# Optimization experiments

Hardware: AMD Instinct MI355X
Metric: run time of the kernel (lower is better)

Reference implementation:

```python
import jax, jax.numpy as jnp
import numpy as np

B, L, D = 4, 2048, 768
K, M, CK = 12, 1, 4            # heads, thetas, conv kernel size
H = D // (K * M)               # 64
DIM_MEM = K * H                # 768
DIM_EXPAND = H * 3             # 192
DSH = DIM_EXPAND * 2           # 384 swiglu head dim
DST = K * DSH                  # 4608
DIM_FUSED = DIM_MEM + K + DST  # 5388
THETA_MIN, THETA_MAX = 1e-3, 3.0


def setup_inputs() -> dict:
    key = jax.random.key(0)
    ks = jax.random.split(key, 5)
    x = jax.random.normal(ks[0], (B, L, D), jnp.float32)
    W_in = jax.random.normal(ks[1], (D, DIM_FUSED), jnp.float32) * 0.02
    conv_w = jax.random.normal(ks[2], (CK, DIM_MEM + K), jnp.float32) * 0.2  # depthwise taps
    rms_scale = jnp.ones((H,), jnp.float32)
    # theta_raw init (M==1 branch): inverse-sigmoid of geomspace grid
    grid = np.geomspace(THETA_MIN, THETA_MAX, K).reshape(1, 1, K, 1, 1)
    base = np.tile(grid, (1, 1, 1, H, 1))
    u = np.clip((base - THETA_MIN) / (THETA_MAX - THETA_MIN), 1e-4, 1 - 1e-4)
    theta_raw = jnp.asarray(np.log(u) - np.log(1.0 - u), jnp.float32)
    decay_slopes = jnp.asarray(np.log(np.exp(np.geomspace(1e-3, 0.1, K)) - 1.0), jnp.float32)
    score_scale = jnp.ones((K,), jnp.float32)
    tanh_scale = jnp.ones((K,), jnp.float32)
    W_sw = jax.random.normal(ks[3], (2 * K * H * M, DST), jnp.float32) * 0.02
    W_out = jax.random.normal(ks[4], (K * DIM_EXPAND, D), jnp.float32) * 0.02
    return {"x": x, "W_in": W_in, "conv_w": conv_w, "rms_scale": rms_scale,
            "theta_raw": theta_raw, "decay_slopes": decay_slopes,
            "score_scale": score_scale, "tanh_scale": tanh_scale,
            "W_sw": W_sw, "W_out": W_out}


def reference(x, W_in, conv_w, rms_scale, theta_raw, decay_slopes,
              score_scale, tanh_scale, W_sw, W_out):
    # fused in-projection
    z_fused = jnp.einsum('bld,df->blf', x, W_in)
    z_mem = z_fused[..., :DIM_MEM + K]
    skip_direct = z_fused[..., DIM_MEM + K:]
    # causal depthwise conv (kernel size CK, left pad CK-1)
    zp = jnp.pad(z_mem, ((0, 0), (CK - 1, 0), (0, 0)))
    z_conv = sum(zp[:, j:j + L, :] * conv_w[j] for j in range(CK))
    z_mem = jax.nn.silu(z_conv)
    # memory keys + RMSNorm over H
    k_val = z_mem[..., :DIM_MEM].reshape(B, L, K, H)
    k_val = k_val * jax.lax.rsqrt(jnp.mean(k_val * k_val, axis=-1, keepdims=True) + 1e-6) * rms_scale
    s_raw = z_mem[..., DIM_MEM:]  # (B, L, K)
    # theta (M == 1)
    theta = THETA_MIN + (THETA_MAX - THETA_MIN) * jax.nn.sigmoid(theta_raw)  # (1,1,K,H,1)
    # decay time weights (num_anchor_heads == 0, maxlen == L)
    pos = jnp.arange(L, dtype=jnp.float32)
    slopes = jax.nn.softplus(decay_slopes).reshape(1, 1, K)
    dist = jnp.maximum(jnp.float32(L - 1) - pos, 0.0)
    log_time_weight = -slopes * dist[None, :, None]  # (1, L, K)
    log_p = jnp.clip(score_scale[None, None, :] * s_raw, -10.0, 10.0)
    p_w = jnp.exp(log_p + log_time_weight)  # (B, L, K)
    # characteristic-function encoding
    k5 = k_val[..., None]  # (B, L, K, H, 1)
    phi = jnp.tanh(k5 * tanh_scale.reshape(1, 1, K, 1, 1)) * theta
    kvw = k5 * p_w[..., None, None]
    re = kvw * jnp.cos(phi)
    im = kvw * jnp.sin(phi)
    # fused causal cumulative accumulation
    flat = K * H * M
    stack = jnp.concatenate([p_w, re.reshape(B, L, flat), im.reshape(B, L, flat)], axis=-1)
    cs = jnp.cumsum(stack, axis=1)
    den_acc = cs[..., :K]
    re_acc = cs[..., K:K + flat].reshape(B, L, K, H, M)
    im_acc = cs[..., K + flat:].reshape(B, L, K, H, M)
    inv_den = (1.0 / jnp.maximum(den_acc, 1e-4))[..., None, None]
    summary_flat = jnp.stack([re_acc * inv_den, im_acc * inv_den], axis=-1).reshape(B, L, -1)
    # SwiGLU with skip
    y_spectral = jnp.einsum('bls,sf->blf', summary_flat, W_sw).reshape(B, L, K, DSH)
    y_skip = skip_direct.reshape(B, L, K, DSH)
    y_spec_val, y_spec_gate = jnp.split(y_spectral, 2, axis=-1)
    y_skip_val, y_skip_gate = jnp.split(y_skip, 2, axis=-1)
    y_act = (y_spec_val + y_skip_val) * jax.nn.silu(y_spec_gate + y_skip_gate)
    out = jnp.einsum('blf,fd->bld', y_act.reshape(B, L, -1), W_out)
    return out
```

## Files before the change

### kernel.cpp

```cpp
#include <hip/hip_runtime.h>
#include <hip/hip_bf16.h>

#define B_       4
#define L_       2048
#define D_       768
#define K_       12
#define H_       64
#define CK_      4
#define DIM_MEM_ 768
#define DMK      780
#define NT       (B_*L_)
#define NSUM     1536
#define NACT     2304
#define NCHUNK   16
#define CHLEN    (L_/NCHUNK)
#define PSTRIDE  132

typedef __attribute__((ext_vector_type(8))) short          bf16x8;
typedef __attribute__((ext_vector_type(8))) unsigned short u16x8;
typedef __attribute__((ext_vector_type(4))) float          f32x4;

__device__ __forceinline__ ushort f2bf(float v) {
    __hip_bfloat16 h = __float2bfloat16(v);
    return *reinterpret_cast<ushort*>(&h);
}
__device__ __forceinline__ float tanh_fast(float x) {
    float t = __expf(-2.f * fabsf(x));
    float r = (1.f - t) / (1.f + t);
    return copysignf(r, x);
}

struct PrepJobs {
    const float* W[6];
    ushort*      out[6];
    int ldw[6], Kd[6], colbase[6], remap[6], ntx[6];
    int start[7];
    const float* cast_in;
    ushort*      cast_out;
    int n4;
};

__global__ __launch_bounds__(256)
void prep_all(PrepJobs J)
{
    int blk = blockIdx.x;
    if (blk >= J.start[6]) {
        int i = (blk - J.start[6]) * 256 + threadIdx.x;
        if (i < J.n4) {
            float4 v = reinterpret_cast<const float4*>(J.cast_in)[i];
            ushort4 o;
            o.x = f2bf(v.x); o.y = f2bf(v.y); o.z = f2bf(v.z); o.w = f2bf(v.w);
            reinterpret_cast<ushort4*>(J.cast_out)[i] = o;
        }
        return;
    }
    int j = 0;
    while (blk >= J.start[j + 1]) ++j;
    int rel = blk - J.start[j];
    int ntx = J.ntx[j];
    int n0 = (rel % ntx) * 32, k0 = (rel / ntx) * 32;
    const float* W = J.W[j];
    int ldw = J.ldw[j], Kd = J.Kd[j], colbase = J.colbase[j], remap = J.remap[j];
    ushort* out = J.out[j];

    __shared__ float tile[32][33];
    int tx = threadIdx.x & 31, ty = threadIdx.x >> 5;
    int n = n0 + tx;
    int c;
    if (remap) {
        int grp = n >> 5, which = (n >> 4) & 1, nn = (grp << 4) + (n & 15);
        c = colbase + (nn / 192) * 384 + which * 192 + (nn % 192);
    } else {
        c = colbase + n;
    }
    #pragma unroll
    for (int r = 0; r < 4; ++r)
        tile[ty + r*8][tx] = W[(size_t)(k0 + ty + r*8) * ldw + c];
    __syncthreads();
    #pragma unroll
    for (int r = 0; r < 4; ++r)
        out[(size_t)(n0 + ty + r*8) * Kd + k0 + tx] = f2bf(tile[tx][ty + r*8]);
}

__global__ __launch_bounds__(256)
void gemm_bf16_mfma(const ushort* __restrict__ A, const ushort* __restrict__ BT,
                    float* __restrict__ C, int Kd, int N, int ldc)
{
    __shared__ ushort As[128*64];
    __shared__ ushort Bs[128*64];
    int tid = threadIdx.x, lane = tid & 63;
    int lr = lane & 15, quad = lane >> 4;
    int wave = tid >> 6;
    int wr = (wave >> 1) * 64, wc = (wave & 1) * 64;
    int m0 = blockIdx.y * 128, n0 = blockIdx.x * 128;

    f32x4 acc[4][4] = {};

    int srow = tid >> 3;
    int tc   = tid & 7;
    const ushort* gA = A  + (size_t)(m0 + srow) * Kd + tc * 8;
    const ushort* gB = BT + (size_t)(n0 + srow) * Kd + tc * 8;
    int woff = srow * 64 + ((tc ^ (srow & 7)) * 8);
    int rx = lr & 7;

    for (int k0 = 0; k0 < Kd; k0 += 64) {
        u16x8 a[4], b[4];
        #pragma unroll
        for (int p = 0; p < 4; ++p) {
            a[p] = *reinterpret_cast<const u16x8*>(gA + (size_t)(32*p) * Kd);
            b[p] = *reinterpret_cast<const u16x8*>(gB + (size_t)(32*p) * Kd);
        }
        gA += 64; gB += 64;
        __syncthreads();
        #pragma unroll
        for (int p = 0; p < 4; ++p) {
            *reinterpret_cast<u16x8*>(As + woff + p*2048) = a[p];
            *reinterpret_cast<u16x8*>(Bs + woff + p*2048) = b[p];
        }
        __syncthreads();
        #pragma unroll
        for (int ks = 0; ks < 2; ++ks) {
            bf16x8 af[4], bf[4];
            #pragma unroll
            for (int i = 0; i < 4; ++i) {
                int ca = ((ks*4 + quad) ^ rx) * 8;
                af[i] = *reinterpret_cast<const bf16x8*>(As + (wr + i*16 + lr) * 64 + ca);
                bf[i] = *reinterpret_cast<const bf16x8*>(Bs + (wc + i*16 + lr) * 64 + ca);
            }
            #pragma unroll
            for (int i = 0; i < 4; ++i)
                #pragma unroll
                for (int j = 0; j < 4; ++j)
                    acc[i][j] = __builtin_amdgcn_mfma_f32_16x16x32_bf16(
                                    af[i], bf[j], acc[i][j], 0, 0, 0);
        }
    }

    #pragma unroll
    for (int i = 0; i < 4; ++i)
        #pragma unroll
        for (int j = 0; j < 4; ++j)
            #pragma unroll
            for (int r = 0; r < 4; ++r) {
                int row = m0 + wr + i*16 + quad*4 + r;
                int col = n0 + wc + j*16 + lr;
                if (col < N)
                    C[(size_t)row * ldc + col] = acc[i][j][r];
            }
}

#define G2NKT 36

#define GLOAD16(gp, dp) __builtin_amdgcn_global_load_lds( \
    (__attribute__((address_space(1))) const void*)(gp),  \
    (__attribute__((address_space(3))) void*)(dp), 16, 0, 0)

__device__ __forceinline__ void g2_stageA(ushort* lds_, int kt,
                                          const ushort* pAs, const ushort* pAx,
                                          int wave, int part)
{
    int ktc = kt > (G2NKT-1) ? (G2NKT-1) : kt;
    const ushort* g; size_t kd;
    if (ktc < 24) { g = pAs + ktc*64;      kd = 1536; }
    else          { g = pAx + (ktc-24)*64; kd = 768;  }
    g += (size_t)(part * 64) * kd;
    ushort* d = lds_ + (kt & 1) * 8192 + part * 4096 + wave * 512;
    GLOAD16(g,           d);
    GLOAD16(g + 32*kd,   d + 2048);
}

__device__ __forceinline__ void g2_stageB(ushort* lds_, int kt,
                                          const ushort* pBs, const ushort* pBx,
                                          int wave)
{
    int ktc = kt > (G2NKT-1) ? (G2NKT-1) : kt;
    const ushort* g; size_t kd;
    if (ktc < 24) { g = pBs + ktc*64;      kd = 1536; }
    else          { g = pBx + (ktc-24)*64; kd = 768;  }
    ushort* d = lds_ + 16384 + (kt & 1) * 12288 + wave * 512;
    #pragma unroll
    for (int s = 0; s < 6; ++s)
        GLOAD16(g + (size_t)(32*s)*kd, d + 2048*s);
}

__global__ __launch_bounds__(256, 2)
void gemm2_2blk(const ushort* __restrict__ Sm, const ushort* __restrict__ Xb,
                const ushort* __restrict__ WsC, const ushort* __restrict__ WiC,
                ushort* __restrict__ yact)
{
    __shared__ ushort lds[40960];
    const int tid  = threadIdx.x;
    const int lane = tid & 63, wave = tid >> 6;
    const int lr = lane & 15, quad = lane >> 4, rx = lr & 7;
    const int wr = (wave >> 1) * 64;
    const int wc = (wave & 1) * 96;
    const int m0 = blockIdx.y * 128, n0 = blockIdx.x * 192;

    const int sr = tid >> 3;
    const int sc = (tid & 7) ^ (sr & 7);
    const ushort* pAs = Sm  + (size_t)(m0 + sr) * 1536 + sc * 8;
    const ushort* pAx = Xb  + (size_t)(m0 + sr) * 768  + sc * 8;
    const ushort* pBs = WsC + (size_t)(n0 + sr) * 1536 + sc * 8;
    const ushort* pBx = WiC + (size_t)(n0 + sr) * 768  + sc * 8;

    f32x4 acc[4][6] = {};
    bf16x8 af[4][2];
    const int ca0 = (quad ^ rx) * 8;
    const int ca1 = ((4 + quad) ^ rx) * 8;

    g2_stageA(lds, 0, pAs, pAx, wave, 0);
    g2_stageA(lds, 0, pAs, pAx, wave, 1);
    g2_stageB(lds, 0, pBs, pBx, wave);
    g2_stageA(lds, 1, pAs, pAx, wave, 0);
    g2_stageA(lds, 1, pAs, pAx, wave, 1);
    asm volatile("s_waitcnt vmcnt(4)" ::: "memory");
    __builtin_amdgcn_s_barrier();

    #pragma unroll 1
    for (int g = 0; g < G2NKT; ++g) {
        const ushort* Ab = lds + (g & 1) * 8192;
        const ushort* Bb = lds + 16384 + (g & 1) * 12288;

        {
            #pragma unroll
            for (int i = 0; i < 4; ++i) {
                const ushort* p = Ab + (wr + i*16 + lr) * 64;
                af[i][0] = *reinterpret_cast<const bf16x8*>(p + ca0);
                af[i][1] = *reinterpret_cast<const bf16x8*>(p + ca1);
            }
            bf16x8 bfr[2][2];
            #pragma unroll
            for (int j = 0; j < 2; ++j) {
                const ushort* p = Bb + (wc + j*16 + lr) * 64;
                bfr[j][0] = *reinterpret_cast<const bf16x8*>(p + ca0);
                bfr[j][1] = *reinterpret_cast<const bf16x8*>(p + ca1);
            }
            g2_stageB(lds, g + 1, pBs, pBx, wave);
            __builtin_amdgcn_s_barrier();
            asm volatile("s_waitcnt lgkmcnt(0)" ::: "memory");
            __builtin_amdgcn_sched_barrier(0);
            __builtin_amdgcn_s_setprio(1);
            #pragma unroll
            for (int ks = 0; ks < 2; ++ks)
                #pragma unroll
                for (int i = 0; i < 4; ++i)
                    #pragma unroll
                    for (int j = 0; j < 2; ++j)
                        acc[i][j] = __builtin_amdgcn_mfma_f32_16x16x32_bf16(
                                        af[i][ks], bfr[j][ks], acc[i][j], 0, 0, 0);
            __builtin_amdgcn_s_setprio(0);
            __builtin_amdgcn_s_barrier();
        }
        {
            bf16x8 bfr[2][2];
            #pragma unroll
            for (int j = 0; j < 2; ++j) {
                const ushort* p = Bb + (wc + (2 + j)*16 + lr) * 64;
                bfr[j][0] = *reinterpret_cast<const bf16x8*>(p + ca0);
                bfr[j][1] = *reinterpret_cast<const bf16x8*>(p + ca1);
            }
            g2_stageA(lds, g + 2, pAs, pAx, wave, 0);
            __builtin_amdgcn_s_barrier();
            asm volatile("s_waitcnt lgkmcnt(0)" ::: "memory");
            __builtin_amdgcn_sched_barrier(0);
            __builtin_amdgcn_s_setprio(1);
            #pragma unroll
            for (int ks = 0; ks < 2; ++ks)
                #pragma unroll
                for (int i = 0; i < 4; ++i)
                    #pragma unroll
                    for (int j = 0; j < 2; ++j)
                        acc[i][2 + j] = __builtin_amdgcn_mfma_f32_16x16x32_bf16(
                                        af[i][ks], bfr[j][ks], acc[i][2 + j], 0, 0, 0);
            __builtin_amdgcn_s_setprio(0);
            __builtin_amdgcn_s_barrier();
        }
        {
            bf16x8 bfr[2][2];
            #pragma unroll
            for (int j = 0; j < 2; ++j) {
                const ushort* p = Bb + (wc + (4 + j)*16 + lr) * 64;
                bfr[j][0] = *reinterpret_cast<const bf16x8*>(p + ca0);
                bfr[j][1] = *reinterpret_cast<const bf16x8*>(p + ca1);
            }
            g2_stageA(lds, g + 2, pAs, pAx, wave, 1);
            asm volatile("s_waitcnt vmcnt(4)" ::: "memory");
            __builtin_amdgcn_s_barrier();
            asm volatile("s_waitcnt lgkmcnt(0)" ::: "memory");
            __builtin_amdgcn_sched_barrier(0);
            __builtin_amdgcn_s_setprio(1);
            #pragma unroll
            for (int ks = 0; ks < 2; ++ks)
                #pragma unroll
                for (int i = 0; i < 4; ++i)
                    #pragma unroll
                    for (int j = 0; j < 2; ++j)
                        acc[i][4 + j] = __builtin_amdgcn_mfma_f32_16x16x32_bf16(
                                        af[i][ks], bfr[j][ks], acc[i][4 + j], 0, 0, 0);
            __builtin_amdgcn_s_setprio(0);
            __builtin_amdgcn_s_barrier();
        }
    }
    asm volatile("s_waitcnt vmcnt(0)" ::: "memory");

    const int vg0 = (n0 + wc) >> 5;
    #pragma unroll
    for (int i = 0; i < 4; ++i)
        #pragma unroll
        for (int p = 0; p < 3; ++p)
            #pragma unroll
            for (int r = 0; r < 4; ++r) {
                int row = m0 + wr + i*16 + quad*4 + r;
                int col = (vg0 + p)*16 + lr;
                float v  = acc[i][2*p][r];
                float gt = acc[i][2*p + 1][r];
                float y = v * (gt / (1.f + __expf(-gt)));
                yact[(size_t)row * NACT + col] = f2bf(y);
            }
}

__global__ __launch_bounds__(256)
void token_kernel(const float* __restrict__ zmem, const float* __restrict__ conv_w,
                  const float* __restrict__ rms_scale, const float* __restrict__ theta_raw,
                  const float* __restrict__ dslopes, const float* __restrict__ sscale,
                  const float* __restrict__ tscale,
                  float* __restrict__ pw, float* __restrict__ re, float* __restrict__ im)
{
    int t = blockIdx.x;
    int b = t >> 11;
    int l = t & (L_ - 1);
    int tid = threadIdx.x;
    int h = tid & 63, kg = tid >> 6;

    __shared__ float s_pw[K_];

    if (tid < K_) {
        float acc = 0.f;
        #pragma unroll
        for (int j = 0; j < CK_; ++j) {
            int ll = l - (CK_ - 1) + j;
            if (ll >= 0)
                acc += zmem[(size_t)(b*L_ + ll)*DMK + DIM_MEM_ + tid]
                     * conv_w[j*DMK + DIM_MEM_ + tid];
        }
        float s  = acc / (1.f + expf(-acc));
        float lp = sscale[tid] * s;
        lp = fminf(10.f, fmaxf(-10.f, lp));
        float slope = log1pf(expf(dslopes[tid]));
        s_pw[tid] = expf(lp - slope * (float)(L_ - 1 - l));
    }

    float kv[3];
    #pragma unroll
    for (int q = 0; q < 3; ++q) {
        int kk = kg + q*4;
        int c = kk*H_ + h;
        float acc = 0.f;
        #pragma unroll
        for (int j = 0; j < CK_; ++j) {
            int ll = l - (CK_ - 1) + j;
            if (ll >= 0)
                acc += zmem[(size_t)(b*L_ + ll)*DMK + c] * conv_w[j*DMK + c];
        }
        kv[q] = acc / (1.f + __expf(-acc));
    }
    __syncthreads();

    #pragma unroll
    for (int q = 0; q < 3; ++q) {
        int kk = kg + q*4;
        float v = kv[q];
        float ss = v * v;
        #pragma unroll
        for (int off = 32; off > 0; off >>= 1)
            ss += __shfl_xor(ss, off, 64);
        float kn = v * rsqrtf(ss * (1.f/64.f) + 1e-6f) * rms_scale[h];
        float th = 0.001f + 2.999f * (1.f / (1.f + __expf(-theta_raw[kk*H_ + h])));
        float phi = tanh_fast(kn * tscale[kk]) * th;
        float kvw = kn * s_pw[kk];
        re[(size_t)t*(K_*H_) + kk*H_ + h] = kvw * __cosf(phi);
        im[(size_t)t*(K_*H_) + kk*H_ + h] = kvw * __sinf(phi);
    }
    if (tid < K_) pw[(size_t)t*K_ + tid] = s_pw[tid];
}

__global__ __launch_bounds__(128)
void scan_sums(const float* __restrict__ pw, const float* __restrict__ re,
               const float* __restrict__ im, float* __restrict__ part)
{
    int blk = blockIdx.x;
    int chunk = blk & (NCHUNK - 1);
    int bk = blk >> 4;
    int k = bk % K_;
    int b = bk / K_;
    int tid = threadIdx.x;
    int h = tid & 63;
    const float* __restrict__ src = (tid >> 6) ? im : re;
    int l0 = chunk * CHLEN;

    size_t base  = ((size_t)(b*L_ + l0))*(K_*H_) + k*H_ + h;
    size_t dbase = ((size_t)(b*L_ + l0))*K_ + k;
    float s = 0.f, ds = 0.f;
    for (int i0 = 0; i0 < CHLEN; i0 += 8) {
        float v[8], d[8];
        #pragma unroll
        for (int j = 0; j < 8; ++j) {
            v[j] = src[base + (size_t)(i0 + j)*(K_*H_)];
            d[j] = pw [dbase + (size_t)(i0 + j)*K_];
        }
        #pragma unroll
        for (int j = 0; j < 8; ++j) { s += v[j]; ds += d[j]; }
    }
    size_t pb = ((size_t)bk * NCHUNK + chunk) * PSTRIDE;
    part[pb + tid] = s;
    if (tid == 0) part[pb + 128] = ds;
}

__global__ __launch_bounds__(128)
void scan_final(const float* __restrict__ pw, const float* __restrict__ re,
                const float* __restrict__ im, const float* __restrict__ part,
                ushort* __restrict__ summary)
{
    int blk = blockIdx.x;
    int chunk = blk & (NCHUNK - 1);
    int bk = blk >> 4;
    int k = bk % K_;
    int b = bk / K_;
    int tid = threadIdx.x;
    int h = tid & 63;
    int pi = tid >> 6;
    const float* __restrict__ src = pi ? im : re;
    int l0 = chunk * CHLEN;

    float acc = 0.f, dacc = 0.f;
    size_t pb0 = (size_t)bk * NCHUNK * PSTRIDE;
    for (int cn = 0; cn < chunk; ++cn) {
        acc  += part[pb0 + (size_t)cn*PSTRIDE + tid];
        dacc += part[pb0 + (size_t)cn*PSTRIDE + 128];
    }

    size_t base  = ((size_t)(b*L_ + l0))*(K_*H_) + k*H_ + h;
    size_t dbase = ((size_t)(b*L_ + l0))*K_ + k;
    int outch = 2*(k*H_ + h) + pi;
    for (int i0 = 0; i0 < CHLEN; i0 += 8) {
        float v[8], d[8];
        #pragma unroll
        for (int j = 0; j < 8; ++j) {
            v[j] = src[base + (size_t)(i0 + j)*(K_*H_)];
            d[j] = pw [dbase + (size_t)(i0 + j)*K_];
        }
        #pragma unroll
        for (int j = 0; j < 8; ++j) {
            acc += v[j]; dacc += d[j];
            float inv = 1.f / fmaxf(dacc, 1e-4f);
            summary[((size_t)(b*L_ + l0 + i0 + j))*NSUM + outch] = f2bf(acc * inv);
        }
    }
}

extern "C" void kernel_launch(void* const* d_in, const int* in_sizes, int n_in,
                              void* d_out, int out_size, void* d_ws, size_t ws_size,
                              hipStream_t stream)
{
    const float* x         = (const float*)d_in[0];
    const float* W_in      = (const float*)d_in[1];
    const float* conv_w    = (const float*)d_in[2];
    const float* rms_scale = (const float*)d_in[3];
    const float* theta_raw = (const float*)d_in[4];
    const float* dslopes   = (const float*)d_in[5];
    const float* sscale    = (const float*)d_in[6];
    const float* tscale    = (const float*)d_in[7];
    const float* W_sw      = (const float*)d_in[8];
    const float* W_out     = (const float*)d_in[9];
    float* out = (float*)d_out;
    char* ws   = (char*)d_ws;

    float*  zmem    = (float*) (ws + 0);
    ushort* summary = (ushort*)(ws + 0);
    float*  pw      = (float*) (ws + 25559040);
    float*  re      = (float*) (ws + 25952256);
    float*  im      = (float*) (ws + 51118080);
    ushort* yact    = (ushort*)(ws + 25952256);
    float*  part    = (float*) (ws + 76283904);
    ushort* xb      = (ushort*)(ws + 76689408);
    ushort* WiCat   = (ushort*)(ws + 89272320);
    ushort* WsCat   = (ushort*)(ws + 96350208);
    ushort* WoT     = (ushort*)(ws + 110505984);
    ushort* WimT    = (ushort*)(ws + 114044928);

    PrepJobs J{};
    J.W[0]=W_in;  J.out[0]=WiCat; J.ldw[0]=5388; J.Kd[0]=768;  J.colbase[0]=780; J.remap[0]=1; J.ntx[0]=144;
    J.W[1]=W_sw;  J.out[1]=WsCat; J.ldw[1]=4608; J.Kd[1]=1536; J.colbase[1]=0;   J.remap[1]=1; J.ntx[1]=144;
    J.W[2]=W_out; J.out[2]=WoT;   J.ldw[2]=768;  J.Kd[2]=2304; J.colbase[2]=0;   J.remap[2]=0; J.ntx[2]=24;
    J.W[3]=W_in;  J.out[3]=WimT;  J.ldw[3]=5388; J.Kd[3]=768;  J.colbase[3]=0;   J.remap[3]=0; J.ntx[3]=28;
    int tiles[4] = {144*24, 144*48, 24*72, 28*24};
    J.start[0] = 0;
    for (int j = 0; j < 4; ++j) J.start[j+1] = J.start[j] + tiles[j];
    J.start[5] = J.start[4];
    J.start[6] = J.start[4];
    J.cast_in = x; J.cast_out = xb; J.n4 = NT*D_/4;
    int nblk = J.start[6] + (J.n4 + 255)/256;

    dim3 blk(256);
    prep_all<<<dim3(nblk), blk, 0, stream>>>(J);
    gemm_bf16_mfma<<<dim3(7, 64), blk, 0, stream>>>(xb, WimT, zmem, 768, 780, 780);
    token_kernel<<<dim3(NT), blk, 0, stream>>>(zmem, conv_w, rms_scale, theta_raw,
                                               dslopes, sscale, tscale, pw, re, im);
    scan_sums <<<dim3(B_*K_*NCHUNK), dim3(128), 0, stream>>>(pw, re, im, part);
    scan_final<<<dim3(B_*K_*NCHUNK), dim3(128), 0, stream>>>(pw, re, im, part, summary);
    gemm2_2blk<<<dim3(24, 64), dim3(256), 0, stream>>>(summary, xb, WsCat, WiCat, yact);
    gemm_bf16_mfma<<<dim3(6, 64), blk, 0, stream>>>(yact, WoT, out, 2304, 768, 768);
}
```

Baseline: 409.7 us.

## Replace three-phase interleaved pipeline in SwiGLU GEMM with single-phase double buffering

The main GEMM loop used to be split into three sub-phases, each with its own barriers and staggered global-to-LDS prefetches. It now issues all prefetches for the next tile up front, reads all A and B fragments from LDS, runs the full MFMA block, then waits on global loads and barriers once per iteration. This removes several barriers per iteration and simplifies the schedule. The cost is shallower prefetch (one tile ahead instead of partly two), a full vmcnt(0) wait on each iteration, and more live B-fragment registers, which could hurt latency hiding or occupancy.

```diff
diff --git a/kernel.cpp b/kernel.cpp
--- a/kernel.cpp
+++ b/kernel.cpp
@@ -184,9 +184,9 @@
 }
 
 __global__ __launch_bounds__(256, 2)
-void gemm2_2blk(const ushort* __restrict__ Sm, const ushort* __restrict__ Xb,
-                const ushort* __restrict__ WsC, const ushort* __restrict__ WiC,
-                ushort* __restrict__ yact)
+void gemm2_1ph(const ushort* __restrict__ Sm, const ushort* __restrict__ Xb,
+               const ushort* __restrict__ WsC, const ushort* __restrict__ WiC,
+               ushort* __restrict__ yact)
 {
     __shared__ ushort lds[40960];
     const int tid  = threadIdx.x;
@@ -204,16 +204,13 @@
     const ushort* pBx = WiC + (size_t)(n0 + sr) * 768  + sc * 8;
 
     f32x4 acc[4][6] = {};
-    bf16x8 af[4][2];
     const int ca0 = (quad ^ rx) * 8;
     const int ca1 = ((4 + quad) ^ rx) * 8;
 
     g2_stageA(lds, 0, pAs, pAx, wave, 0);
     g2_stageA(lds, 0, pAs, pAx, wave, 1);
     g2_stageB(lds, 0, pBs, pBx, wave);
-    g2_stageA(lds, 1, pAs, pAx, wave, 0);
-    g2_stageA(lds, 1, pAs, pAx, wave, 1);
-    asm volatile("s_waitcnt vmcnt(4)" ::: "memory");
+    asm volatile("s_waitcnt vmcnt(0)" ::: "memory");
     __builtin_amdgcn_s_barrier();
 
     #pragma unroll 1
@@ -221,87 +218,37 @@
         const ushort* Ab = lds + (g & 1) * 8192;
         const ushort* Bb = lds + 16384 + (g & 1) * 12288;
 
-        {
+        g2_stageA(lds, g + 1, pAs, pAx, wave, 0);
+        g2_stageA(lds, g + 1, pAs, pAx, wave, 1);
+        g2_stageB(lds, g + 1, pBs, pBx, wave);
+
+        bf16x8 af[4][2], bfr[6][2];
+        #pragma unroll
+        for (int i = 0; i < 4; ++i) {
+            const ushort* p = Ab + (wr + i*16 + lr) * 64;
+            af[i][0] = *reinterpret_cast<const bf16x8*>(p + ca0);
+            af[i][1] = *reinterpret_cast<const bf16x8*>(p + ca1);
+        }
+        #pragma unroll
+        for (int j = 0; j < 6; ++j) {
+            const ushort* p = Bb + (wc + j*16 + lr) * 64;
+            bfr[j][0] = *reinterpret_cast<const bf16x8*>(p + ca0);
+            bfr[j][1] = *reinterpret_cast<const bf16x8*>(p + ca1);
+        }
+        __builtin_amdgcn_s_setprio(1);
+        #pragma unroll
+        for (int ks = 0; ks < 2; ++ks)
             #pragma unroll
-            for (int i = 0; i < 4; ++i) {
-                const ushort* p = Ab + (wr + i*16 + lr) * 64;
-                af[i][0] = *reinterpret_cast<const bf16x8*>(p + ca0);
-                af[i][1] = *reinterpret_cast<const bf16x8*>(p + ca1);
-            }
-            bf16x8 bfr[2][2];
-            #pragma unroll
-            for (int j = 0; j < 2; ++j) {
-                const ushort* p = Bb + (wc + j*16 + lr) * 64;
-                bfr[j][0] = *reinterpret_cast<const bf16x8*>(p + ca0);
-                bfr[j][1] = *reinterpret_cast<const bf16x8*>(p + ca1);
-            }
-            g2_stageB(lds, g + 1, pBs, pBx, wave);
-            __builtin_amdgcn_s_barrier();
-            asm volatile("s_waitcnt lgkmcnt(0)" ::: "memory");
-            __builtin_amdgcn_sched_barrier(0);
-            __builtin_amdgcn_s_setprio(1);
-            #pragma unroll
-            for (int ks = 0; ks < 2; ++ks)
+            for (int i = 0; i < 4; ++i)
                 #pragma unroll
-                for (int i = 0; i < 4; ++i)
-                    #pragma unroll
-                    for (int j = 0; j < 2; ++j)
-                        acc[i][j] = __builtin_amdgcn_mfma_f32_16x16x32_bf16(
-                                        af[i][ks], bfr[j][ks], acc[i][j], 0, 0, 0);
-            __builtin_amdgcn_s_setprio(0);
-            __builtin_amdgcn_s_barrier();
-        }
-        {
-            bf16x8 bfr[2][2];
-            #pragma unroll
-            for (int j = 0; j < 2; ++j) {
-                const ushort* p = Bb + (wc + (2 + j)*16 + lr) * 64;
-                bfr[j][0] = *reinterpret_cast<const bf16x8*>(p + ca0);
-                bfr[j][1] = *reinterpret_cast<const bf16x8*>(p + ca1);
-            }
-            g2_stageA(lds, g + 2, pAs, pAx, wave, 0);
-            __builtin_amdgcn_s_barrier();
-            asm volatile("s_waitcnt lgkmcnt(0)" ::: "memory");
-            __builtin_amdgcn_sched_barrier(0);
-            __builtin_amdgcn_s_setprio(1);
-            #pragma unroll
-            for (int ks = 0; ks < 2; ++ks)
-                #pragma unroll
-                for (int i = 0; i < 4; ++i)
-                    #pragma unroll
-                    for (int j = 0; j < 2; ++j)
-                        acc[i][2 + j] = __builtin_amdgcn_mfma_f32_16x16x32_bf16(
-                                        af[i][ks], bfr[j][ks], acc[i][2 + j], 0, 0, 0);
-            __builtin_amdgcn_s_setprio(0);
-            __builtin_amdgcn_s_barrier();
-        }
-        {
-            bf16x8 bfr[2][2];
-            #pragma unroll
-            for (int j = 0; j < 2; ++j) {
-                const ushort* p = Bb + (wc + (4 + j)*16 + lr) * 64;
-                bfr[j][0] = *reinterpret_cast<const bf16x8*>(p + ca0);
-                bfr[j][1] = *reinterpret_cast<const bf16x8*>(p + ca1);
-            }
-            g2_stageA(lds, g + 2, pAs, pAx, wave, 1);
-            asm volatile("s_waitcnt vmcnt(4)" ::: "memory");
-            __builtin_amdgcn_s_barrier();
-            asm volatile("s_waitcnt lgkmcnt(0)" ::: "memory");
-            __builtin_amdgcn_sched_barrier(0);
-            __builtin_amdgcn_s_setprio(1);
-            #pragma unroll
-            for (int ks = 0; ks < 2; ++ks)
-                #pragma unroll
-                for (int i = 0; i < 4; ++i)
-                    #pragma unroll
-                    for (int j = 0; j < 2; ++j)
-                        acc[i][4 + j] = __builtin_amdgcn_mfma_f32_16x16x32_bf16(
-                                        af[i][ks], bfr[j][ks], acc[i][4 + j], 0, 0, 0);
-            __builtin_amdgcn_s_setprio(0);
-            __builtin_amdgcn_s_barrier();
-        }
-    }
-    asm volatile("s_waitcnt vmcnt(0)" ::: "memory");
+                for (int j = 0; j < 6; ++j)
+                    acc[i][j] = __builtin_amdgcn_mfma_f32_16x16x32_bf16(
+                                    af[i][ks], bfr[j][ks], acc[i][j], 0, 0, 0);
+        __builtin_amdgcn_s_setprio(0);
+
+        asm volatile("s_waitcnt vmcnt(0)" ::: "memory");
+        __builtin_amdgcn_s_barrier();
+    }
 
     const int vg0 = (n0 + wc) >> 5;
     #pragma unroll
@@ -508,6 +455,6 @@
                                                dslopes, sscale, tscale, pw, re, im);
     scan_sums <<<dim3(B_*K_*NCHUNK), dim3(128), 0, stream>>>(pw, re, im, part);
     scan_final<<<dim3(B_*K_*NCHUNK), dim3(128), 0, stream>>>(pw, re, im, part, summary);
-    gemm2_2blk<<<dim3(24, 64), dim3(256), 0, stream>>>(summary, xb, WsCat, WiCat, yact);
+    gemm2_1ph<<<dim3(24, 64), dim3(256), 0, stream>>>(summary, xb, WsCat, WiCat, yact);
     gemm_bf16_mfma<<<dim3(6, 64), blk, 0, stream>>>(yact, WoT, out, 2304, 768, 768);
 }
```

After: 418.3 us. +2.1%, slower.
